# Performance work log

Measured on AMD Instinct MI355X. Metric: run time of the kernel, lower is better.

Reference implementation:

```python
import jax, jax.numpy as jnp
import numpy as np

C = 256
NUM_GROUPS = 32
EPS = 1e-5


def group_norm(x, gamma, beta):
    # x: [B, C, H, W]; normalize within each of NUM_GROUPS channel groups
    B, Cc, H, W = x.shape
    xg = x.reshape(B, NUM_GROUPS, Cc // NUM_GROUPS, H, W)
    mean = xg.mean(axis=(2, 3, 4), keepdims=True)
    var = xg.var(axis=(2, 3, 4), keepdims=True)
    xg = (xg - mean) * jax.lax.rsqrt(var + EPS)
    x = xg.reshape(B, Cc, H, W)
    return x * gamma[None, :, None, None] + beta[None, :, None, None]


def conv1x1(x, w, b):
    # w: [C_out, C_in], b: [C_out]; equivalent to nn.Conv2d(k=1)
    return jnp.einsum('oc,bchw->bohw', w, x) + b[None, :, None, None]


def setup_inputs() -> dict:
    key = jax.random.key(0)
    ks = jax.random.split(key, 12)
    B, H, W = 8, 64, 64
    x = jax.random.normal(ks[0], (B, C, H, W), dtype=jnp.float32)
    temb = jax.random.normal(ks[1], (B, 512), dtype=jnp.float32)
    s = 1.0 / np.sqrt(C)  # kaiming-uniform-ish scale for 1x1 conv
    def wmat(k):
        return jax.random.uniform(k, (C, C), dtype=jnp.float32, minval=-s, maxval=s)
    def bvec(k):
        return jax.random.uniform(k, (C,), dtype=jnp.float32, minval=-s, maxval=s)
    return {
        'x': x, 'temb': temb,
        'gn_w': jnp.ones((C,), jnp.float32), 'gn_b': jnp.zeros((C,), jnp.float32),
        'wq': wmat(ks[2]), 'bq': bvec(ks[3]),
        'wk': wmat(ks[4]), 'bk': bvec(ks[5]),
        'wv': wmat(ks[6]), 'bv': bvec(ks[7]),
        'wp': wmat(ks[8]), 'bp': bvec(ks[9]),
    }


def reference(x, temb, gn_w, gn_b, wq, bq, wk, bk, wv, bv, wp, bp):
    B, Cc, H, W = x.shape
    h = group_norm(x, gn_w, gn_b)
    q = conv1x1(h, wq, bq)
    k = conv1x1(h, wk, bk)
    v = conv1x1(h, wv, bv)
    # full self-attention over spatial positions: scores [B, H, W, H, W]
    scale = Cc ** (-0.5)
    w = jnp.einsum('bchw,bcij->bhwij', q, k) * scale
    w = jax.nn.softmax(w.reshape(B, H, W, H * W), axis=-1).reshape(B, H, W, H, W)
    h = jnp.einsum('bhwij,bcij->bchw', w, v)
    h = conv1x1(h, wp, bp)
    return (x + h, temb)
```

## Files before the change

### kernel.cpp

```cpp
#include <hip/hip_runtime.h>
#include <hip/hip_bf16.h>

#define B_ 8
#define C_ 256
#define S_ 4096
#define G_ 32
#define GC_ 8
#define EPS_ 1e-5f

typedef __attribute__((ext_vector_type(4))) float f32x4;
typedef __attribute__((ext_vector_type(8))) short bf16x8;
typedef __attribute__((ext_vector_type(4))) short bf16x4;
typedef __attribute__((ext_vector_type(4))) unsigned int u32x4;
typedef __attribute__((ext_vector_type(2))) unsigned int u32x2;

#define DI __device__ __forceinline__

DI unsigned short f2bf(float f) {
    union { float f; unsigned u; } v; v.f = f;
    unsigned r = v.u + 0x7fffu + ((v.u >> 16) & 1u);
    return (unsigned short)(r >> 16);
}

DI unsigned cvt_pk_bf16(float lo, float hi) {
    unsigned r;
    asm("v_cvt_pk_bf16_f32 %0, %1, %2" : "=v"(r) : "v"(lo), "v"(hi));
    return r;
}

DI unsigned cvt_pk_fp8(float lo, float hi) {
    unsigned r;
    asm("v_cvt_pk_fp8_f32 %0, %1, %2" : "=v"(r) : "v"(lo), "v"(hi));
    return r;
}

DI f32x4 mfma_fp8(u32x2 a, u32x2 b, f32x4 c) {
    union { u32x2 u; long l; } ua, ub;
    ua.u = a; ub.u = b;
    return __builtin_amdgcn_mfma_f32_16x16x32_fp8_fp8(ua.l, ub.l, c, 0, 0, 0);
}

__global__ __launch_bounds__(256) void k_gn_stats(const float* __restrict__ x,
                                                  float* __restrict__ stats) {
    int bg = blockIdx.x;
    const float4* xp = (const float4*)(x + (size_t)bg * (GC_ * S_));
    float s = 0.f, ss = 0.f;
    for (int i = threadIdx.x; i < GC_ * S_ / 4; i += 256) {
        float4 v = xp[i];
        s  += v.x + v.y + v.z + v.w;
        ss += v.x * v.x + v.y * v.y + v.z * v.z + v.w * v.w;
    }
    #pragma unroll
    for (int off = 32; off; off >>= 1) { s += __shfl_down(s, off); ss += __shfl_down(ss, off); }
    __shared__ float rs[4], rss[4];
    int w = threadIdx.x >> 6;
    if ((threadIdx.x & 63) == 0) { rs[w] = s; rss[w] = ss; }
    __syncthreads();
    if (threadIdx.x == 0) {
        float S1 = rs[0] + rs[1] + rs[2] + rs[3];
        float S2 = rss[0] + rss[1] + rss[2] + rss[3];
        float inv = 1.f / (GC_ * S_);
        float mean = S1 * inv;
        float var = S2 * inv - mean * mean;
        stats[bg * 2] = mean;
        stats[bg * 2 + 1] = rsqrtf(var + EPS_);
    }
}

__global__ __launch_bounds__(256) void k_gn_apply(const float* __restrict__ x,
                                                  const float* __restrict__ stats,
                                                  const float* __restrict__ gw,
                                                  const float* __restrict__ gb,
                                                  unsigned short* __restrict__ h) {
    int b = blockIdx.x >> 6;
    int s0 = (blockIdx.x & 63) * 64;
    __shared__ unsigned short tile[64 * 256];
    const float* xb = x + (size_t)b * C_ * S_;
    for (int id = threadIdx.x; id < 256 * 16; id += 256) {
        int c = id >> 4, s4 = id & 15;
        float4 v = *(const float4*)(xb + (size_t)c * S_ + s0 + s4 * 4);
        float mean = stats[(b * G_ + (c >> 3)) * 2];
        float rstd = stats[(b * G_ + (c >> 3)) * 2 + 1];
        float ga = gw[c], be = gb[c];
        float vv[4] = {v.x, v.y, v.z, v.w};
        #pragma unroll
        for (int i = 0; i < 4; i++) {
            int srow = s4 * 4 + i;
            unsigned byte = srow * 512u + c * 2u;
            byte ^= ((srow & 7u) << 4);
            *(unsigned short*)((char*)tile + byte) = f2bf((vv[i] - mean) * rstd * ga + be);
        }
    }
    __syncthreads();
    unsigned short* hb = h + (size_t)b * S_ * C_;
    for (int id = threadIdx.x; id < 2048; id += 256) {
        int srow = id >> 5, ck = id & 31;
        unsigned byte = srow * 512u + ck * 16u;
        byte ^= ((srow & 7u) << 4);
        u32x4 v = *(u32x4*)((char*)tile + byte);
        *(u32x4*)(hb + (size_t)(s0 + srow) * C_ + ck * 8) = v;
    }
}

__global__ __launch_bounds__(256) void k_wcvt(const float* __restrict__ wq, const float* __restrict__ wk,
                                              const float* __restrict__ wv, const float* __restrict__ wp,
                                              unsigned short* __restrict__ wbf) {
    int t = blockIdx.x * 256 + threadIdx.x;
    int mat = t >> 13;
    int idx = (t & 8191) * 8;
    const float* src = mat == 0 ? wq : mat == 1 ? wk : mat == 2 ? wv : wp;
    float4 a = *(const float4*)(src + idx);
    float4 c = *(const float4*)(src + idx + 4);
    unsigned short tmp[8] = {f2bf(a.x), f2bf(a.y), f2bf(a.z), f2bf(a.w),
                             f2bf(c.x), f2bf(c.y), f2bf(c.z), f2bf(c.w)};
    *(u32x4*)(wbf + mat * 65536 + idx) = *(u32x4*)tmp;
}

__global__ __launch_bounds__(256) void k_qkv(const unsigned short* __restrict__ wbf,
                                             const float* __restrict__ bq,
                                             const float* __restrict__ bk,
                                             const float* __restrict__ bv,
                                             const unsigned short* __restrict__ h,
                                             unsigned char* __restrict__ q8,
                                             unsigned char* __restrict__ k8,
                                             unsigned char* __restrict__ v8) {
    int mode = blockIdx.x >> 9;
    int inner = blockIdx.x & 511;
    int b = inner & 7;
    int rest = inner >> 3;
    int m0 = (rest & 1) * 128;
    int n0 = (rest >> 1) * 128;
    const unsigned short* W = wbf + mode * 65536;
    const float* bias = mode == 0 ? bq : (mode == 1 ? bk : bv);

    __shared__ unsigned short Alds[128 * 64];
    __shared__ unsigned short Blds[128 * 64];
    int tid = threadIdx.x;
    int lane = tid & 63, wv = tid >> 6;
    int wm = (wv >> 1) * 64, wn = (wv & 1) * 64;
    int lr = lane & 15, lg = lane >> 4;
    f32x4 acc[4][4] = {};
    const unsigned short* Bb = h + (size_t)b * S_ * C_;

    for (int k0 = 0; k0 < 256; k0 += 64) {
        __syncthreads();
        #pragma unroll
        for (int i = 0; i < 4; i++) {
            int id = tid + i * 256;
            int row = id >> 3, ck = id & 7;
            u32x4 v = *(const u32x4*)(W + (size_t)(m0 + row) * C_ + k0 + ck * 8);
            unsigned byte = row * 128u + ck * 16u;
            byte ^= ((row & 7u) << 4);
            *(u32x4*)((char*)Alds + byte) = v;
        }
        #pragma unroll
        for (int i = 0; i < 4; i++) {
            int id = tid + i * 256;
            int row = id >> 3, ck = id & 7;
            u32x4 v = *(const u32x4*)(Bb + (size_t)(n0 + row) * C_ + k0 + ck * 8);
            unsigned byte = row * 128u + ck * 16u;
            byte ^= ((row & 7u) << 4);
            *(u32x4*)((char*)Blds + byte) = v;
        }
        __syncthreads();
        #pragma unroll
        for (int ks = 0; ks < 2; ks++) {
            bf16x8 af[4], bf[4];
            #pragma unroll
            for (int mf = 0; mf < 4; mf++) {
                int m = wm + mf * 16 + lr;
                unsigned byte = m * 128u + ks * 64u + lg * 16u;
                byte ^= ((m & 7u) << 4);
                af[mf] = *(bf16x8*)((char*)Alds + byte);
            }
            #pragma unroll
            for (int nf = 0; nf < 4; nf++) {
                int n = wn + nf * 16 + lr;
                unsigned byte = n * 128u + ks * 64u + lg * 16u;
                byte ^= ((n & 7u) << 4);
                bf[nf] = *(bf16x8*)((char*)Blds + byte);
            }
            #pragma unroll
            for (int mf = 0; mf < 4; mf++)
                #pragma unroll
                for (int nf = 0; nf < 4; nf++)
                    acc[mf][nf] = __builtin_amdgcn_mfma_f32_16x16x32_bf16(af[mf], bf[nf], acc[mf][nf], 0, 0, 0);
        }
    }

    if (mode < 2) {
        unsigned char* ob = (mode == 0 ? q8 : k8) + (size_t)b * S_ * C_;
        #pragma unroll
        for (int mf = 0; mf < 4; mf++)
            #pragma unroll
            for (int nf = 0; nf < 4; nf++) {
                int cbase = m0 + wm + mf * 16 + lg * 4;
                int srow = n0 + wn + nf * 16 + lr;
                float v0 = acc[mf][nf][0] + bias[cbase + 0];
                float v1 = acc[mf][nf][1] + bias[cbase + 1];
                float v2 = acc[mf][nf][2] + bias[cbase + 2];
                float v3 = acc[mf][nf][3] + bias[cbase + 3];
                unsigned lo = cvt_pk_fp8(v0, v1);
                unsigned hi = cvt_pk_fp8(v2, v3);
                *(unsigned*)(ob + (size_t)srow * C_ + cbase) = (lo & 0xffffu) | (hi << 16);
            }
    } else {
        unsigned char* ob = v8 + (size_t)b * C_ * S_;
        #pragma unroll
        for (int mf = 0; mf < 4; mf++)
            #pragma unroll
            for (int nf = 0; nf < 4; nf++)
                #pragma unroll
                for (int r = 0; r < 4; r++) {
                    int c = m0 + wm + mf * 16 + lg * 4 + r;
                    int s = n0 + wn + nf * 16 + lr;
                    ob[(size_t)c * S_ + s] = (unsigned char)(cvt_pk_fp8(acc[mf][nf][r] + bias[c], 0.f) & 0xffu);
                }
    }
}

__global__ __launch_bounds__(256) void k_proj(const unsigned short* __restrict__ wbf,
                                              const float* __restrict__ bias,
                                              const unsigned short* __restrict__ Bm,
                                              float* __restrict__ outf,
                                              const float* __restrict__ xres) {
    int b = blockIdx.x & 7;
    int rest = blockIdx.x >> 3;
    int m0 = (rest & 1) * 128;
    int n0 = (rest >> 1) * 128;
    const unsigned short* W = wbf + 3 * 65536;

    __shared__ unsigned short Alds[128 * 64];
    __shared__ unsigned short Blds[128 * 64];
    int tid = threadIdx.x;
    int lane = tid & 63, wv = tid >> 6;
    int wm = (wv >> 1) * 64, wn = (wv & 1) * 64;
    int lr = lane & 15, lg = lane >> 4;
    f32x4 acc[4][4] = {};
    const unsigned short* Bb = Bm + (size_t)b * S_ * C_;

    for (int k0 = 0; k0 < 256; k0 += 64) {
        __syncthreads();
        #pragma unroll
        for (int i = 0; i < 4; i++) {
            int id = tid + i * 256;
            int row = id >> 3, ck = id & 7;
            u32x4 v = *(const u32x4*)(W + (size_t)(m0 + row) * C_ + k0 + ck * 8);
            unsigned byte = row * 128u + ck * 16u;
            byte ^= ((row & 7u) << 4);
            *(u32x4*)((char*)Alds + byte) = v;
        }
        #pragma unroll
        for (int i = 0; i < 4; i++) {
            int id = tid + i * 256;
            int row = id >> 3, ck = id & 7;
            u32x4 v = *(const u32x4*)(Bb + (size_t)(n0 + row) * C_ + k0 + ck * 8);
            unsigned byte = row * 128u + ck * 16u;
            byte ^= ((row & 7u) << 4);
            *(u32x4*)((char*)Blds + byte) = v;
        }
        __syncthreads();
        #pragma unroll
        for (int ks = 0; ks < 2; ks++) {
            bf16x8 af[4], bf[4];
            #pragma unroll
            for (int mf = 0; mf < 4; mf++) {
                int m = wm + mf * 16 + lr;
                unsigned byte = m * 128u + ks * 64u + lg * 16u;
                byte ^= ((m & 7u) << 4);
                af[mf] = *(bf16x8*)((char*)Alds + byte);
            }
            #pragma unroll
            for (int nf = 0; nf < 4; nf++) {
                int n = wn + nf * 16 + lr;
                unsigned byte = n * 128u + ks * 64u + lg * 16u;
                byte ^= ((n & 7u) << 4);
                bf[nf] = *(bf16x8*)((char*)Blds + byte);
            }
            #pragma unroll
            for (int mf = 0; mf < 4; mf++)
                #pragma unroll
                for (int nf = 0; nf < 4; nf++)
                    acc[mf][nf] = __builtin_amdgcn_mfma_f32_16x16x32_bf16(af[mf], bf[nf], acc[mf][nf], 0, 0, 0);
        }
    }

    const float* xb = xres + (size_t)b * C_ * S_;
    #pragma unroll
    for (int mf = 0; mf < 4; mf++)
        #pragma unroll
        for (int nf = 0; nf < 4; nf++)
            #pragma unroll
            for (int r = 0; r < 4; r++) {
                int c = m0 + wm + mf * 16 + lg * 4 + r;
                int s = n0 + wn + nf * 16 + lr;
                outf[(size_t)b * C_ * S_ + (size_t)c * S_ + s] =
                    acc[mf][nf][r] + bias[c] + xb[(size_t)c * S_ + s];
            }
}

__global__ __launch_bounds__(512, 2) void k_attn(const unsigned char* __restrict__ Q8,
                                                 const unsigned char* __restrict__ K8,
                                                 const unsigned char* __restrict__ V8,
                                                 unsigned short* __restrict__ O) {
    int b = blockIdx.x & 7;
    int q0 = (blockIdx.x >> 3) * 128;
    int tid = threadIdx.x, lane = tid & 63, wv = tid >> 6;
    int lr = lane & 15, lg = lane >> 4;
    int qg = wv & 3, kg = wv >> 2;
    int qw = q0 + qg * 32;
    __shared__ unsigned char Klds8[64 * 256];
    __shared__ unsigned char Vlds8[256 * 72];
    __shared__ unsigned char Plds8[4][32 * 72];
    __shared__ float mlp[8 * 2 * 16];
    const unsigned char* Qb = Q8 + (size_t)b * S_ * C_;
    const unsigned char* Kb = K8 + (size_t)b * S_ * C_;
    const unsigned char* Vb = V8 + (size_t)b * C_ * S_;

    const float QS = 0.09016844f;

    u32x2 qf8[8][2];
    #pragma unroll
    for (int ks = 0; ks < 8; ks++)
        #pragma unroll
        for (int qf = 0; qf < 2; qf++)
            qf8[ks][qf] = *(const u32x2*)(Qb + (size_t)(qw + qf * 16 + lr) * C_ + ks * 32 + lg * 8);

    unsigned kaddr[2][8];
    #pragma unroll
    for (int kf = 0; kf < 2; kf++) {
        int key = kg * 32 + kf * 16 + lr;
        #pragma unroll
        for (int ks = 0; ks < 8; ks++)
            kaddr[kf][ks] = (unsigned)key * 256u + (((unsigned)(4 * ks + lg + 2 * key) & 31u) << 3);
    }
    unsigned vbase[2];
    vbase[0] = (unsigned)(kg * 128 + lr) * 72u + lg * 8u;
    vbase[1] = vbase[0] + 32u;

    f32x4 acc[8][2] = {};
    float lrun[2] = {0.f, 0.f};

    int kr0[2], kc16[2], vc[4], vk8[4];
    #pragma unroll
    for (int i = 0; i < 2; i++) {
        int id = tid + i * 512;
        kr0[i] = id >> 4; kc16[i] = id & 15;
    }
    #pragma unroll
    for (int i = 0; i < 4; i++) {
        int id = tid + i * 512;
        vc[i] = id >> 3;  vk8[i] = id & 7;
    }
    unsigned kwb[2], vwb[4];
    #pragma unroll
    for (int i = 0; i < 2; i++)
        kwb[i] = kr0[i] * 256u + (((unsigned)(2 * kc16[i] + 2 * kr0[i]) & 31u) << 3);
    #pragma unroll
    for (int i = 0; i < 4; i++)
        vwb[i] = vc[i] * 72u + vk8[i] * 8u;

    u32x4 kpre[2];
    u32x2 vpre[4];
    #pragma unroll
    for (int i = 0; i < 2; i++)
        kpre[i] = *(const u32x4*)(Kb + (size_t)kr0[i] * C_ + kc16[i] * 16);
    #pragma unroll
    for (int i = 0; i < 4; i++)
        vpre[i] = *(const u32x2*)(Vb + (size_t)vc[i] * S_ + vk8[i] * 8);
    #pragma unroll
    for (int i = 0; i < 2; i++)
        *(u32x4*)(Klds8 + kwb[i]) = kpre[i];
    #pragma unroll
    for (int i = 0; i < 4; i++)
        *(u32x2*)(Vlds8 + vwb[i]) = vpre[i];
    __syncthreads();

    for (int kt = 0; kt < 64; kt++) {
        bool pf = (kt + 1) < 64;
        if (pf) {
            #pragma unroll
            for (int i = 0; i < 2; i++)
                kpre[i] = *(const u32x4*)(Kb + (size_t)((kt + 1) * 64 + kr0[i]) * C_ + kc16[i] * 16);
        }

        f32x4 sc[2][2] = {};
        #pragma unroll
        for (int ks = 0; ks < 8; ks++) {
            u32x2 a0 = *(const u32x2*)(Klds8 + kaddr[0][ks]);
            u32x2 a1 = *(const u32x2*)(Klds8 + kaddr[1][ks]);
            sc[0][0] = mfma_fp8(a0, qf8[ks][0], sc[0][0]);
            sc[0][1] = mfma_fp8(a0, qf8[ks][1], sc[0][1]);
            sc[1][0] = mfma_fp8(a1, qf8[ks][0], sc[1][0]);
            sc[1][1] = mfma_fp8(a1, qf8[ks][1], sc[1][1]);
        }

        #pragma unroll
        for (int qf = 0; qf < 2; qf++)
            #pragma unroll
            for (int kf = 0; kf < 2; kf++) {
                float p0 = __builtin_amdgcn_exp2f(fmaf(sc[kf][qf][0], QS, -2.f));
                float p1 = __builtin_amdgcn_exp2f(fmaf(sc[kf][qf][1], QS, -2.f));
                float p2 = __builtin_amdgcn_exp2f(fmaf(sc[kf][qf][2], QS, -2.f));
                float p3 = __builtin_amdgcn_exp2f(fmaf(sc[kf][qf][3], QS, -2.f));
                lrun[qf] += (p0 + p1) + (p2 + p3);
                unsigned pk = (cvt_pk_fp8(p0, p1) & 0xffffu) | (cvt_pk_fp8(p2, p3) << 16);
                int q = qf * 16 + lr;
                *(unsigned*)(&Plds8[qg][0] + (unsigned)q * 72u + kg * 32u + kf * 16u + lg * 4u) = pk;
            }

        if (pf) {
            #pragma unroll
            for (int i = 0; i < 4; i++)
                vpre[i] = *(const u32x2*)(Vb + (size_t)vc[i] * S_ + (kt + 1) * 64 + vk8[i] * 8);
        }

        __syncthreads();

        if (pf) {
            #pragma unroll
            for (int i = 0; i < 2; i++)
                *(u32x4*)(Klds8 + kwb[i]) = kpre[i];
        }

        #pragma unroll
        for (int ks2 = 0; ks2 < 2; ks2++) {
            u32x2 pb[2];
            #pragma unroll
            for (int qf = 0; qf < 2; qf++) {
                int q = qf * 16 + lr;
                pb[qf] = *(const u32x2*)(&Plds8[qg][0] + (unsigned)q * 72u + ks2 * 32u + lg * 8u);
            }
            #pragma unroll
            for (int cf = 0; cf < 8; cf++) {
                u32x2 va = *(const u32x2*)(Vlds8 + vbase[ks2] + cf * 1152u);
                #pragma unroll
                for (int qf = 0; qf < 2; qf++)
                    acc[cf][qf] = mfma_fp8(va, pb[qf], acc[cf][qf]);
            }
        }

        __syncthreads();

        if (pf) {
            #pragma unroll
            for (int i = 0; i < 4; i++)
                *(u32x2*)(Vlds8 + vwb[i]) = vpre[i];
        }
    }

    float ls[2];
    #pragma unroll
    for (int qf = 0; qf < 2; qf++) {
        float t = lrun[qf];
        t += __shfl_xor(t, 16);
        t += __shfl_xor(t, 32);
        ls[qf] = t;
    }
    if (lg == 0) {
        #pragma unroll
        for (int qf = 0; qf < 2; qf++) mlp[(wv * 2 + qf) * 16 + lr] = ls[qf];
    }
    __syncthreads();
    unsigned short* Ob = O + (size_t)b * S_ * C_;
    #pragma unroll
    for (int qf = 0; qf < 2; qf++) {
        float inv = 1.f / (ls[qf] + mlp[((wv ^ 4) * 2 + qf) * 16 + lr]);
        int srow = qw + qf * 16 + lr;
        #pragma unroll
        for (int cf = 0; cf < 8; cf++) {
            u32x2 pk;
            pk[0] = cvt_pk_bf16(acc[cf][qf][0] * inv, acc[cf][qf][1] * inv);
            pk[1] = cvt_pk_bf16(acc[cf][qf][2] * inv, acc[cf][qf][3] * inv);
            *(u32x2*)(Ob + (size_t)srow * C_ + kg * 128 + cf * 16 + lg * 4) = pk;
        }
    }
}

__global__ __launch_bounds__(256) void k_copy_temb(const float* __restrict__ t, float* __restrict__ o) {
    int i = blockIdx.x * 256 + threadIdx.x;
    if (i < B_ * 512) o[i] = t[i];
}

extern "C" void kernel_launch(void* const* d_in, const int* in_sizes, int n_in,
                              void* d_out, int out_size, void* d_ws, size_t ws_size,
                              hipStream_t stream) {
    (void)in_sizes; (void)n_in; (void)out_size; (void)ws_size;
    const float* x  = (const float*)d_in[0];
    const float* temb = (const float*)d_in[1];
    const float* gw = (const float*)d_in[2];
    const float* gb = (const float*)d_in[3];
    const float* wq = (const float*)d_in[4];
    const float* bq = (const float*)d_in[5];
    const float* wk = (const float*)d_in[6];
    const float* bk = (const float*)d_in[7];
    const float* wv = (const float*)d_in[8];
    const float* bv = (const float*)d_in[9];
    const float* wp = (const float*)d_in[10];
    const float* bp = (const float*)d_in[11];
    float* out = (float*)d_out;

    char* ws = (char*)d_ws;
    const size_t MB = 1024 * 1024;
    unsigned short* h_sc = (unsigned short*)ws;
    unsigned char*  v8   = (unsigned char*)(ws + 16 * MB);
    unsigned char*  q8   = (unsigned char*)(ws + 24 * MB);
    unsigned char*  k8   = (unsigned char*)(ws + 32 * MB);
    float* stats = (float*)(ws + 40 * MB);
    unsigned short* wbf = (unsigned short*)(ws + 40 * MB + 4096);

    k_wcvt<<<128, 256, 0, stream>>>(wq, wk, wv, wp, wbf);
    k_gn_stats<<<B_ * G_, 256, 0, stream>>>(x, stats);
    k_gn_apply<<<B_ * (S_ / 64), 256, 0, stream>>>(x, stats, gw, gb, h_sc);
    k_qkv<<<1536, 256, 0, stream>>>(wbf, bq, bk, bv, h_sc, q8, k8, v8);
    k_attn<<<B_ * (S_ / 128), 512, 0, stream>>>(q8, k8, v8, h_sc);
    k_proj<<<512, 256, 0, stream>>>(wbf, bp, h_sc, out, x);
    k_copy_temb<<<(B_ * 512 + 255) / 256, 256, 0, stream>>>(temb, out + (size_t)B_ * C_ * S_);
}
```

Baseline: 193.5 us.

## Halve attention query tile and split keys and channels across four wave groups

The attention kernel now processes 64 queries per block instead of 128, with 2 query groups by 4 key/channel groups of waves. Each wave computes 16 keys of scores and 64 output channels, so per-wave accumulators shrink and launch bounds ask for 4 blocks per CU. The grid doubles, raising occupancy and parallelism for the 256-CU device. In exchange each block reloads the full K/V stream for half as many queries, doubling K/V global and LDS traffic per unit of work. The row-sum reduction now combines four partial sums.

```diff
diff --git a/kernel.cpp b/kernel.cpp
--- a/kernel.cpp
+++ b/kernel.cpp
@@ -299,19 +299,19 @@
             }
 }
 
-__global__ __launch_bounds__(512, 2) void k_attn(const unsigned char* __restrict__ Q8,
+__global__ __launch_bounds__(512, 4) void k_attn(const unsigned char* __restrict__ Q8,
                                                  const unsigned char* __restrict__ K8,
                                                  const unsigned char* __restrict__ V8,
                                                  unsigned short* __restrict__ O) {
     int b = blockIdx.x & 7;
-    int q0 = (blockIdx.x >> 3) * 128;
+    int q0 = (blockIdx.x >> 3) * 64;
     int tid = threadIdx.x, lane = tid & 63, wv = tid >> 6;
     int lr = lane & 15, lg = lane >> 4;
-    int qg = wv & 3, kg = wv >> 2;
+    int qg = wv & 1, kg = wv >> 1;
     int qw = q0 + qg * 32;
     __shared__ unsigned char Klds8[64 * 256];
     __shared__ unsigned char Vlds8[256 * 72];
-    __shared__ unsigned char Plds8[4][32 * 72];
+    __shared__ unsigned char Plds8[2][32 * 72];
     __shared__ float mlp[8 * 2 * 16];
     const unsigned char* Qb = Q8 + (size_t)b * S_ * C_;
     const unsigned char* Kb = K8 + (size_t)b * S_ * C_;
@@ -326,19 +326,18 @@
         for (int qf = 0; qf < 2; qf++)
             qf8[ks][qf] = *(const u32x2*)(Qb + (size_t)(qw + qf * 16 + lr) * C_ + ks * 32 + lg * 8);
 
-    unsigned kaddr[2][8];
-    #pragma unroll
-    for (int kf = 0; kf < 2; kf++) {
-        int key = kg * 32 + kf * 16 + lr;
+    unsigned kaddr[8];
+    {
+        int key = kg * 16 + lr;
         #pragma unroll
         for (int ks = 0; ks < 8; ks++)
-            kaddr[kf][ks] = (unsigned)key * 256u + (((unsigned)(4 * ks + lg + 2 * key) & 31u) << 3);
+            kaddr[ks] = (unsigned)key * 256u + (((unsigned)(4 * ks + lg + 2 * key) & 31u) << 3);
     }
     unsigned vbase[2];
-    vbase[0] = (unsigned)(kg * 128 + lr) * 72u + lg * 8u;
+    vbase[0] = (unsigned)(kg * 64 + lr) * 72u + lg * 8u;
     vbase[1] = vbase[0] + 32u;
 
-    f32x4 acc[8][2] = {};
+    f32x4 acc[4][2] = {};
     float lrun[2] = {0.f, 0.f};
 
     int kr0[2], kc16[2], vc[4], vk8[4];
@@ -384,30 +383,25 @@
                 kpre[i] = *(const u32x4*)(Kb + (size_t)((kt + 1) * 64 + kr0[i]) * C_ + kc16[i] * 16);
         }
 
-        f32x4 sc[2][2] = {};
+        f32x4 sc[2] = {};
         #pragma unroll
         for (int ks = 0; ks < 8; ks++) {
-            u32x2 a0 = *(const u32x2*)(Klds8 + kaddr[0][ks]);
-            u32x2 a1 = *(const u32x2*)(Klds8 + kaddr[1][ks]);
-            sc[0][0] = mfma_fp8(a0, qf8[ks][0], sc[0][0]);
-            sc[0][1] = mfma_fp8(a0, qf8[ks][1], sc[0][1]);
-            sc[1][0] = mfma_fp8(a1, qf8[ks][0], sc[1][0]);
-            sc[1][1] = mfma_fp8(a1, qf8[ks][1], sc[1][1]);
-        }
-
-        #pragma unroll
-        for (int qf = 0; qf < 2; qf++)
-            #pragma unroll
-            for (int kf = 0; kf < 2; kf++) {
-                float p0 = __builtin_amdgcn_exp2f(fmaf(sc[kf][qf][0], QS, -2.f));
-                float p1 = __builtin_amdgcn_exp2f(fmaf(sc[kf][qf][1], QS, -2.f));
-                float p2 = __builtin_amdgcn_exp2f(fmaf(sc[kf][qf][2], QS, -2.f));
-                float p3 = __builtin_amdgcn_exp2f(fmaf(sc[kf][qf][3], QS, -2.f));
-                lrun[qf] += (p0 + p1) + (p2 + p3);
-                unsigned pk = (cvt_pk_fp8(p0, p1) & 0xffffu) | (cvt_pk_fp8(p2, p3) << 16);
-                int q = qf * 16 + lr;
-                *(unsigned*)(&Plds8[qg][0] + (unsigned)q * 72u + kg * 32u + kf * 16u + lg * 4u) = pk;
-            }
+            u32x2 a = *(const u32x2*)(Klds8 + kaddr[ks]);
+            sc[0] = mfma_fp8(a, qf8[ks][0], sc[0]);
+            sc[1] = mfma_fp8(a, qf8[ks][1], sc[1]);
+        }
+
+        #pragma unroll
+        for (int qf = 0; qf < 2; qf++) {
+            float p0 = __builtin_amdgcn_exp2f(fmaf(sc[qf][0], QS, -2.f));
+            float p1 = __builtin_amdgcn_exp2f(fmaf(sc[qf][1], QS, -2.f));
+            float p2 = __builtin_amdgcn_exp2f(fmaf(sc[qf][2], QS, -2.f));
+            float p3 = __builtin_amdgcn_exp2f(fmaf(sc[qf][3], QS, -2.f));
+            lrun[qf] += (p0 + p1) + (p2 + p3);
+            unsigned pk = (cvt_pk_fp8(p0, p1) & 0xffffu) | (cvt_pk_fp8(p2, p3) << 16);
+            int q = qf * 16 + lr;
+            *(unsigned*)(&Plds8[qg][0] + (unsigned)q * 72u + kg * 16u + lg * 4u) = pk;
+        }
 
         if (pf) {
             #pragma unroll
@@ -432,7 +426,7 @@
                 pb[qf] = *(const u32x2*)(&Plds8[qg][0] + (unsigned)q * 72u + ks2 * 32u + lg * 8u);
             }
             #pragma unroll
-            for (int cf = 0; cf < 8; cf++) {
+            for (int cf = 0; cf < 4; cf++) {
                 u32x2 va = *(const u32x2*)(Vlds8 + vbase[ks2] + cf * 1152u);
                 #pragma unroll
                 for (int qf = 0; qf < 2; qf++)
@@ -465,14 +459,16 @@
     unsigned short* Ob = O + (size_t)b * S_ * C_;
     #pragma unroll
     for (int qf = 0; qf < 2; qf++) {
-        float inv = 1.f / (ls[qf] + mlp[((wv ^ 4) * 2 + qf) * 16 + lr]);
+        float lt = mlp[((qg + 0) * 2 + qf) * 16 + lr] + mlp[((qg + 2) * 2 + qf) * 16 + lr]
+                 + mlp[((qg + 4) * 2 + qf) * 16 + lr] + mlp[((qg + 6) * 2 + qf) * 16 + lr];
+        float inv = 1.f / lt;
         int srow = qw + qf * 16 + lr;
         #pragma unroll
-        for (int cf = 0; cf < 8; cf++) {
+        for (int cf = 0; cf < 4; cf++) {
             u32x2 pk;
             pk[0] = cvt_pk_bf16(acc[cf][qf][0] * inv, acc[cf][qf][1] * inv);
             pk[1] = cvt_pk_bf16(acc[cf][qf][2] * inv, acc[cf][qf][3] * inv);
-            *(u32x2*)(Ob + (size_t)srow * C_ + kg * 128 + cf * 16 + lg * 4) = pk;
+            *(u32x2*)(Ob + (size_t)srow * C_ + kg * 64 + cf * 16 + lg * 4) = pk;
         }
     }
 }
@@ -513,7 +509,7 @@
     k_gn_stats<<<B_ * G_, 256, 0, stream>>>(x, stats);
     k_gn_apply<<<B_ * (S_ / 64), 256, 0, stream>>>(x, stats, gw, gb, h_sc);
     k_qkv<<<1536, 256, 0, stream>>>(wbf, bq, bk, bv, h_sc, q8, k8, v8);
-    k_attn<<<B_ * (S_ / 128), 512, 0, stream>>>(q8, k8, v8, h_sc);
+    k_attn<<<B_ * (S_ / 64), 512, 0, stream>>>(q8, k8, v8, h_sc);
     k_proj<<<512, 256, 0, stream>>>(wbf, bp, h_sc, out, x);
     k_copy_temb<<<(B_ * 512 + 255) / 256, 256, 0, stream>>>(temb, out + (size_t)B_ * C_ * S_);
 }
```

Result: slower. 200.5 us (+3.6%).
